# Kernel tuning notes

Measured on AMD Instinct MI355X. Metric: run time of the kernel, lower is better.

Reference implementation:

```python
import jax, jax.numpy as jnp
import numpy as np

IN_F = 4096
OUT_F = 4096
RANK = 16
TOKENS = 8192
WORDS = IN_F // 16  # 16 int2 codes per int32 word
LORA_SCALE = 1.0


def pack_int2(codes):
    """codes: [out_f, in_f] int32 in {0,1,2} -> packed [out_f, in_f//16] int32.
    Little-endian: code k of a word sits at bits [2k, 2k+1]."""
    c = codes.reshape(codes.shape[0], -1, 16)  # [out, words, 16]
    shifts = jnp.arange(16, dtype=jnp.int32) * 2
    return jnp.sum(c << shifts, axis=-1).astype(jnp.int32)


def unpack_int2(packed, in_features):
    """packed: [out_f, words] int32 -> ternary floats [out_f, in_f] in {-1,0,+1}."""
    shifts = jnp.arange(16, dtype=jnp.int32) * 2
    codes = (packed[:, :, None] >> shifts) & 3  # [out, words, 16]
    codes = codes.reshape(packed.shape[0], -1)[:, :in_features]
    return codes - 1  # {0,1,2} -> {-1,0,+1}


def setup_inputs() -> dict:
    key = jax.random.key(0)
    kx, kc, ka, km, kb, kA, kB = jax.random.split(key, 7)
    x = jax.random.normal(kx, (TOKENS, IN_F), dtype=jnp.float32)
    codes = jax.random.randint(kc, (OUT_F, IN_F), 0, 3, dtype=jnp.int32)  # {0,1,2}
    int2_packed = pack_int2(codes)  # [OUT_F, WORDS]
    alpha = jax.random.uniform(ka, (OUT_F,), dtype=jnp.float32) * 0.1 + 0.01
    mu = jax.random.normal(km, (OUT_F,), dtype=jnp.float32) * 0.01
    bias = jax.random.normal(kb, (OUT_F,), dtype=jnp.float32) * 0.02
    lora_A = jax.random.normal(kA, (RANK, IN_F), dtype=jnp.float32) * 0.02
    lora_B = jax.random.normal(kB, (OUT_F, RANK), dtype=jnp.float32) * 0.02
    return {"x": x, "int2_packed": int2_packed, "alpha": alpha, "mu": mu,
            "bias": bias, "lora_A": lora_A, "lora_B": lora_B}


def reference(x, int2_packed, alpha, mu, bias, lora_A, lora_B):
    # Unpack ternary weight T in {-1,0,+1}: [OUT_F, IN_F]
    T = unpack_int2(int2_packed, IN_F).astype(x.dtype)
    # ternary matmul, per-row scale alpha
    out = jnp.einsum('ti,oi->to', x, T) * alpha[None, :]
    # asymmetric shift: mu_o * sum_i x_i
    out = out + mu[None, :] * jnp.sum(x, axis=-1, keepdims=True)
    # LoRA correction: scale * (x A^T) B^T
    lora_out = jnp.einsum('tr,or->to', jnp.einsum('ti,ri->tr', x, lora_A), lora_B)
    out = out + LORA_SCALE * lora_out
    return out + bias[None, :]
```

## Files before the change

kernel.cpp:

```cpp
#include <hip/hip_runtime.h>
#include <stdint.h>

#define IN_F   4096
#define OUT_F  4096
#define TOKENS 8192
#define RANK   16

#define BM 128
#define BN 128
#define BKI 64

typedef unsigned short u16;
typedef __attribute__((ext_vector_type(8))) short bf16x8;
typedef __attribute__((ext_vector_type(4))) float f32x4;
typedef __attribute__((ext_vector_type(4))) int i32x4;

#define GLDS16(g, l) __builtin_amdgcn_global_load_lds( \
    (__attribute__((address_space(1))) void*)(g),      \
    (__attribute__((address_space(3))) void*)(l), 16, 0, 0)

__device__ __forceinline__ int swz_row(int row) {
    return (row & 3) ^ ((row >> 2) & 1);
}

__device__ __forceinline__ u16 bf16bits(float f) {
    unsigned int u = __builtin_bit_cast(unsigned int, f);
    unsigned int lsb = (u >> 16) & 1u;
    u += 0x7fffu + lsb;
    return (u16)(u >> 16);
}

__device__ __forceinline__ unsigned int quant4(float a, float b, float c, float d, float inv) {
    int qa = __float2int_rn(a * inv); qa = max(-127, min(127, qa));
    int qb = __float2int_rn(b * inv); qb = max(-127, min(127, qb));
    int qc = __float2int_rn(c * inv); qc = max(-127, min(127, qc));
    int qd = __float2int_rn(d * inv); qd = max(-127, min(127, qd));
    return (qa & 255) | ((qb & 255) << 8) | ((qc & 255) << 16) | ((qd & 255) << 24);
}

__global__ __launch_bounds__(256) void k_prep(const float* __restrict__ X,
                                              const int* __restrict__ packed,
                                              const float* __restrict__ lA,
                                              const float* __restrict__ lB,
                                              signed char* __restrict__ Xq,
                                              float* __restrict__ sArr,
                                              float* __restrict__ SArr,
                                              signed char* __restrict__ Wq,
                                              u16* __restrict__ Bl,
                                              signed char* __restrict__ Aq,
                                              float* __restrict__ aScale) {
    __shared__ float rs[4], rm[4];
    const int b = blockIdx.x;
    const int tid = threadIdx.x;
    const int lane = tid & 63;
    const int wv = tid >> 6;

    if (b < TOKENS) {
        const int t = b;
        const float4* X4 = (const float4*)(X + (size_t)t * IN_F);
        float4 v[4];
#pragma unroll
        for (int j = 0; j < 4; j++) v[j] = X4[tid * 4 + j];

        float s = 0.f, m = 0.f;
#pragma unroll
        for (int j = 0; j < 4; j++) {
            s += v[j].x + v[j].y + v[j].z + v[j].w;
            m = fmaxf(m, fmaxf(fmaxf(fabsf(v[j].x), fabsf(v[j].y)),
                               fmaxf(fabsf(v[j].z), fabsf(v[j].w))));
        }
#pragma unroll
        for (int off = 32; off > 0; off >>= 1) {
            s += __shfl_down(s, off);
            m = fmaxf(m, __shfl_down(m, off));
        }
        if (lane == 0) { rs[wv] = s; rm[wv] = m; }
        __syncthreads();
        float S = rs[0] + rs[1] + rs[2] + rs[3];
        float M = fmaxf(fmaxf(rm[0], rm[1]), fmaxf(rm[2], rm[3]));
        M = fmaxf(M, 1e-20f);
        if (tid == 0) { SArr[t] = S; sArr[t] = M / 127.0f; }

        float inv = 127.0f / M;
        uint4 o;
        o.x = quant4(v[0].x, v[0].y, v[0].z, v[0].w, inv);
        o.y = quant4(v[1].x, v[1].y, v[1].z, v[1].w, inv);
        o.z = quant4(v[2].x, v[2].y, v[2].z, v[2].w, inv);
        o.w = quant4(v[3].x, v[3].y, v[3].z, v[3].w, inv);
        *(uint4*)(Xq + (size_t)t * IN_F + tid * 16) = o;
    } else if (b < TOKENS + OUT_F * (IN_F / 16) / 256) {
        int idx = (b - TOKENS) * 256 + tid;
        int p = packed[idx];
        uint4 o;
        unsigned int w[4];
#pragma unroll
        for (int g = 0; g < 4; g++) {
            unsigned int word = 0;
#pragma unroll
            for (int j = 0; j < 4; j++) {
                int k = g * 4 + j;
                int bb = ((p >> (2 * k)) & 3) - 1;
                word |= (unsigned int)(bb & 255) << (8 * j);
            }
            w[g] = word;
        }
        o.x = w[0]; o.y = w[1]; o.z = w[2]; o.w = w[3];
        *(uint4*)(Wq + (size_t)idx * 16) = o;
    } else if (b < TOKENS + OUT_F * (IN_F / 16) / 256 + OUT_F / 256) {
        int o = (b - TOKENS - OUT_F * (IN_F / 16) / 256) * 256 + tid;
        const float4* B4 = (const float4*)(lB + (size_t)o * RANK);
        float4 b0 = B4[0], b1 = B4[1], b2 = B4[2], b3 = B4[3];
        union { u16 u[32]; uint4 q[4]; } ob;
        ob.u[0] = bf16bits(b0.x); ob.u[1] = bf16bits(b0.y); ob.u[2] = bf16bits(b0.z); ob.u[3] = bf16bits(b0.w);
        ob.u[4] = bf16bits(b1.x); ob.u[5] = bf16bits(b1.y); ob.u[6] = bf16bits(b1.z); ob.u[7] = bf16bits(b1.w);
        ob.u[8] = bf16bits(b2.x); ob.u[9] = bf16bits(b2.y); ob.u[10] = bf16bits(b2.z); ob.u[11] = bf16bits(b2.w);
        ob.u[12] = bf16bits(b3.x); ob.u[13] = bf16bits(b3.y); ob.u[14] = bf16bits(b3.z); ob.u[15] = bf16bits(b3.w);
#pragma unroll
        for (int k = 16; k < 32; k++) ob.u[k] = 0;
        uint4* dst = (uint4*)(Bl + (size_t)o * 32);
        dst[0] = ob.q[0]; dst[1] = ob.q[1]; dst[2] = ob.q[2]; dst[3] = ob.q[3];
    } else {
        const int r = b - (TOKENS + OUT_F * (IN_F / 16) / 256 + OUT_F / 256);
        const float4* A4 = (const float4*)(lA + (size_t)r * IN_F);
        float4 v[4];
#pragma unroll
        for (int j = 0; j < 4; j++) v[j] = A4[tid * 4 + j];

        float m = 0.f;
#pragma unroll
        for (int j = 0; j < 4; j++)
            m = fmaxf(m, fmaxf(fmaxf(fabsf(v[j].x), fabsf(v[j].y)),
                               fmaxf(fabsf(v[j].z), fabsf(v[j].w))));
#pragma unroll
        for (int off = 32; off > 0; off >>= 1) m = fmaxf(m, __shfl_down(m, off));
        if (lane == 0) rm[wv] = m;
        __syncthreads();
        float M = fmaxf(fmaxf(rm[0], rm[1]), fmaxf(rm[2], rm[3]));
        M = fmaxf(M, 1e-20f);
        if (tid == 0) aScale[r] = M / 127.0f;

        float inv = 127.0f / M;
        uint4 o;
        o.x = quant4(v[0].x, v[0].y, v[0].z, v[0].w, inv);
        o.y = quant4(v[1].x, v[1].y, v[1].z, v[1].w, inv);
        o.z = quant4(v[2].x, v[2].y, v[2].z, v[2].w, inv);
        o.w = quant4(v[3].x, v[3].y, v[3].z, v[3].w, inv);
        *(uint4*)(Aq + (size_t)r * IN_F + tid * 16) = o;
    }
}

__global__ __launch_bounds__(256) void k_lora_y(const signed char* __restrict__ Xq,
                                                const signed char* __restrict__ Aq,
                                                const float* __restrict__ sArr,
                                                const float* __restrict__ aScale,
                                                u16* __restrict__ ypad) {
    __shared__ i32x4 red[4][64];
    const int tid = threadIdx.x;
    const int lane = tid & 63;
    const int wv = tid >> 6;
    const int t0 = blockIdx.x * 16;
    const int fr = lane & 15;
    const int q16 = (lane >> 4) * 16;

    i32x4 acc = {};
    const signed char* xrow = Xq + (size_t)(t0 + fr) * IN_F + wv * 1024 + q16;
    const signed char* arow = Aq + (size_t)fr * IN_F + wv * 1024 + q16;
#pragma unroll
    for (int k0 = 0; k0 < 1024; k0 += BKI) {
        i32x4 af = *(const i32x4*)(xrow + k0);
        i32x4 bf = *(const i32x4*)(arow + k0);
        acc = __builtin_amdgcn_mfma_i32_16x16x64_i8(af, bf, acc, 0, 0, 0);
    }
    red[wv][lane] = acc;
    __syncthreads();
    if (wv == 0) {
        i32x4 s0 = red[0][lane], s1 = red[1][lane], s2 = red[2][lane], s3 = red[3][lane];
        const int c0 = lane & 15;
        const int r0 = (lane >> 4) * 4;
        float asc = aScale[c0];
#pragma unroll
        for (int r = 0; r < 4; r++) {
            int t = t0 + r0 + r;
            float y = sArr[t] * asc * (float)(s0[r] + s1[r] + s2[r] + s3[r]);
            ypad[(size_t)t * 32 + c0] = bf16bits(y);
            ypad[(size_t)t * 32 + 16 + c0] = 0;
        }
    }
}

__global__ __launch_bounds__(256, 2) void k_gemm_i8(const signed char* __restrict__ Xq,
                                                    const signed char* __restrict__ Wq,
                                                    const float* __restrict__ sArr,
                                                    const float* __restrict__ SArr,
                                                    const float* __restrict__ alpha,
                                                    const float* __restrict__ mu,
                                                    const float* __restrict__ bias,
                                                    const u16* __restrict__ ypad,
                                                    const u16* __restrict__ Bl,
                                                    float* __restrict__ out) {
    __shared__ unsigned char smem[16384];
    unsigned char* smA = smem;
    unsigned char* smB = smem + 8192;

    const int tid = threadIdx.x;
    const int lane = tid & 63;
    const int wv = tid >> 6;
    const int wm = (wv >> 1) * 64;
    const int wn = (wv & 1) * 64;
    const int fr = lane & 15;
    const int qs = lane >> 4;
    const int sw = swz_row(fr);
    const int rdoff = ((qs ^ sw) << 4);
    const int wvbase = wv * 1024;

    const int m0 = blockIdx.y * BM;
    const int n0 = blockIdx.x * BN;

    int srow[2], soff[2];
#pragma unroll
    for (int i = 0; i < 2; i++) {
        int c = i * 256 + tid;
        srow[i] = c >> 2;
        soff[i] = (((c & 3) ^ swz_row(c >> 2)) << 4);
    }

    i32x4 acc[4][4] = {};

    for (int k0 = 0; k0 < IN_F; k0 += BKI) {
        __syncthreads();
#pragma unroll
        for (int i = 0; i < 2; i++)
            GLDS16(Xq + (size_t)(m0 + srow[i]) * IN_F + k0 + soff[i], smA + i * 4096 + wvbase);
#pragma unroll
        for (int i = 0; i < 2; i++)
            GLDS16(Wq + (size_t)(n0 + srow[i]) * IN_F + k0 + soff[i], smB + i * 4096 + wvbase);
        __syncthreads();

        i32x4 af[4], bf[4];
#pragma unroll
        for (int mt = 0; mt < 4; mt++)
            af[mt] = *(const i32x4*)(smA + (wm + mt * 16 + fr) * BKI + rdoff);
#pragma unroll
        for (int nt = 0; nt < 4; nt++)
            bf[nt] = *(const i32x4*)(smB + (wn + nt * 16 + fr) * BKI + rdoff);
#pragma unroll
        for (int mt = 0; mt < 4; mt++)
#pragma unroll
            for (int nt = 0; nt < 4; nt++)
                acc[mt][nt] = __builtin_amdgcn_mfma_i32_16x16x64_i8(af[mt], bf[nt], acc[mt][nt], 0, 0, 0);
    }

    const int r0 = (lane >> 4) * 4;
    const int c0 = lane & 15;
    f32x4 facc[4][4];
#pragma unroll
    for (int mt = 0; mt < 4; mt++) {
        int rb = m0 + wm + mt * 16 + r0;
        f32x4 sv = *(const f32x4*)(sArr + rb);
        f32x4 Sv = *(const f32x4*)(SArr + rb);
#pragma unroll
        for (int nt = 0; nt < 4; nt++) {
            int col = n0 + wn + nt * 16 + c0;
            float av = alpha[col], mv = mu[col], bv = bias[col];
#pragma unroll
            for (int r = 0; r < 4; r++)
                facc[mt][nt][r] = av * sv[r] * (float)acc[mt][nt][r] + fmaf(mv, Sv[r], bv);
        }
    }

    __syncthreads();
#pragma unroll
    for (int i = 0; i < 2; i++) {
        GLDS16((const unsigned char*)ypad + (size_t)(m0 + srow[i]) * 64 + soff[i], smA + i * 4096 + wvbase);
        GLDS16((const unsigned char*)Bl + (size_t)(n0 + srow[i]) * 64 + soff[i], smB + i * 4096 + wvbase);
    }
    __syncthreads();
    bf16x8 yf[4], blf[4];
#pragma unroll
    for (int mt = 0; mt < 4; mt++)
        yf[mt] = *(const bf16x8*)(smA + (wm + mt * 16 + fr) * 64 + rdoff);
#pragma unroll
    for (int nt = 0; nt < 4; nt++)
        blf[nt] = *(const bf16x8*)(smB + (wn + nt * 16 + fr) * 64 + rdoff);
#pragma unroll
    for (int mt = 0; mt < 4; mt++)
#pragma unroll
        for (int nt = 0; nt < 4; nt++)
            facc[mt][nt] = __builtin_amdgcn_mfma_f32_16x16x32_bf16(yf[mt], blf[nt], facc[mt][nt], 0, 0, 0);

#pragma unroll
    for (int nt = 0; nt < 4; nt++) {
        int col = n0 + wn + nt * 16 + c0;
#pragma unroll
        for (int mt = 0; mt < 4; mt++) {
            int row = m0 + wm + mt * 16 + r0;
            float* op = out + (size_t)row * OUT_F + col;
#pragma unroll
            for (int r = 0; r < 4; r++)
                op[(size_t)r * OUT_F] = facc[mt][nt][r];
        }
    }
}

extern "C" void kernel_launch(void* const* d_in, const int* in_sizes, int n_in,
                              void* d_out, int out_size, void* d_ws, size_t ws_size,
                              hipStream_t stream) {
    const float* x      = (const float*)d_in[0];
    const int*   packed = (const int*)d_in[1];
    const float* alpha  = (const float*)d_in[2];
    const float* mu     = (const float*)d_in[3];
    const float* bias   = (const float*)d_in[4];
    const float* lA     = (const float*)d_in[5];
    const float* lB     = (const float*)d_in[6];
    float* out = (float*)d_out;

    char* p = (char*)d_ws;
    signed char* Wq = (signed char*)p;             p += (size_t)OUT_F * IN_F;
    signed char* Xq = (signed char*)p;             p += (size_t)TOKENS * IN_F;
    float* sArr = (float*)p;                       p += (size_t)TOKENS * 4;
    float* SArr = (float*)p;                       p += (size_t)TOKENS * 4;
    u16* ypad = (u16*)p;                           p += (size_t)TOKENS * 32 * 2;
    u16* Bl = (u16*)p;                             p += (size_t)OUT_F * 32 * 2;
    signed char* Aq = (signed char*)p;             p += (size_t)RANK * IN_F;
    float* aScale = (float*)p;                     p += RANK * 4;

    const int prep_blocks = TOKENS + OUT_F * (IN_F / 16) / 256 + OUT_F / 256 + RANK;
    k_prep<<<dim3(prep_blocks), dim3(256), 0, stream>>>(x, packed, lA, lB, Xq, sArr, SArr, Wq, Bl, Aq, aScale);
    k_lora_y<<<dim3(TOKENS / 16), dim3(256), 0, stream>>>(Xq, Aq, sArr, aScale, ypad);

    dim3 grid(OUT_F / BN, TOKENS / BM);
    k_gemm_i8<<<grid, dim3(256), 0, stream>>>(Xq, Wq, sArr, SArr, alpha, mu, bias, ypad, Bl, out);
}
```

Baseline: 395.5 us.

## Rewrite int8 GEMM as 256x256 tile, 8-wave, double-buffered ping-pong pipeline

The int8 GEMM moves from 128x128 tiles with a 64-deep K step and single-buffered LDS to 256x256 tiles with a 128-deep K step and 512 threads. It double-buffers 128KB of LDS, splits each K tile into half-tile phases that overlap global-to-LDS loads with MFMA work, and uses explicit vmcnt waits, barriers and setprio. A swizzled 1D grid improves L2 locality. The aim is to hide memory latency and raise MFMA utilisation, at the cost of large LDS use (likely one block per CU despite the launch bound) and more register pressure.

```diff
diff --git a/kernel.cpp b/kernel.cpp
--- a/kernel.cpp
+++ b/kernel.cpp
@@ -6,9 +6,10 @@
 #define TOKENS 8192
 #define RANK   16
 
-#define BM 128
-#define BN 128
-#define BKI 64
+#define BM 256
+#define BN 256
+#define BK 128
+#define NT (IN_F / BK)
 
 typedef unsigned short u16;
 typedef __attribute__((ext_vector_type(8))) short bf16x8;
@@ -19,9 +20,12 @@
     (__attribute__((address_space(1))) void*)(g),      \
     (__attribute__((address_space(3))) void*)(l), 16, 0, 0)
 
-__device__ __forceinline__ int swz_row(int row) {
-    return (row & 3) ^ ((row >> 2) & 1);
-}
+#define MEMFENCE asm volatile("" ::: "memory")
+#define BARRIER  do { MEMFENCE; __builtin_amdgcn_s_barrier(); MEMFENCE; } while (0)
+#define VMCNT8   asm volatile("s_waitcnt vmcnt(8)" ::: "memory")
+#define VMCNT0   asm volatile("s_waitcnt vmcnt(0)" ::: "memory")
+
+__device__ __forceinline__ int swz4(int row) { return (row & 3) ^ ((row >> 2) & 1); }
 
 __device__ __forceinline__ u16 bf16bits(float f) {
     unsigned int u = __builtin_bit_cast(unsigned int, f);
@@ -166,7 +170,7 @@
     const signed char* xrow = Xq + (size_t)(t0 + fr) * IN_F + wv * 1024 + q16;
     const signed char* arow = Aq + (size_t)fr * IN_F + wv * 1024 + q16;
 #pragma unroll
-    for (int k0 = 0; k0 < 1024; k0 += BKI) {
+    for (int k0 = 0; k0 < 1024; k0 += 64) {
         i32x4 af = *(const i32x4*)(xrow + k0);
         i32x4 bf = *(const i32x4*)(arow + k0);
         acc = __builtin_amdgcn_mfma_i32_16x16x64_i8(af, bf, acc, 0, 0, 0);
@@ -188,7 +192,80 @@
     }
 }
 
-__global__ __launch_bounds__(256, 2) void k_gemm_i8(const signed char* __restrict__ Xq,
+
+#define STAGE_A(srcTile, h, dbuf)                                              \
+    {                                                                          \
+        _Pragma("unroll")                                                      \
+        for (int j = 0; j < 2; j++) {                                          \
+            int c = j * 512 + tid;                                             \
+            int rho = c >> 3;                                                  \
+            int sl = (c & 7) ^ (rho & 7);                                      \
+            int trow = ((rho >> 6) << 7) + ((h) << 6) + (rho & 63);            \
+            GLDS16(Xq + (size_t)(m0 + trow) * IN_F + (srcTile) * BK + sl * 16, \
+                   smem + (dbuf) * 65536 + (h) * 16384 + j * 8192 + wvb);      \
+        }                                                                      \
+    }
+
+#define STAGE_B(srcTile, h, dbuf)                                              \
+    {                                                                          \
+        _Pragma("unroll")                                                      \
+        for (int j = 0; j < 2; j++) {                                          \
+            int c = j * 512 + tid;                                             \
+            int rho = c >> 3;                                                  \
+            int sl = (c & 7) ^ (rho & 7);                                      \
+            int tcol = ((rho >> 5) << 6) + ((h) << 5) + (rho & 31);            \
+            GLDS16(Wq + (size_t)(n0 + tcol) * IN_F + (srcTile) * BK + sl * 16, \
+                   smem + (dbuf) * 65536 + 32768 + (h) * 16384 + j * 8192 + wvb); \
+        }                                                                      \
+    }
+
+#define READ_A(h)                                                              \
+    {                                                                          \
+        _Pragma("unroll")                                                      \
+        for (int ml = 0; ml < 4; ml++) {                                       \
+            _Pragma("unroll")                                                  \
+            for (int ks = 0; ks < 2; ks++) {                                   \
+                int rho = wmi * 64 + ml * 16 + fr;                             \
+                int s = (ks * 4 + qs) ^ (rho & 7);                             \
+                af[ml][ks] = *(const i32x4*)(smem + d * 65536 + (h) * 16384 +  \
+                                             rho * 128 + s * 16);              \
+            }                                                                  \
+        }                                                                      \
+    }
+
+#define READ_B(hb)                                                             \
+    {                                                                          \
+        _Pragma("unroll")                                                      \
+        for (int nl = 0; nl < 2; nl++) {                                       \
+            _Pragma("unroll")                                                  \
+            for (int ks = 0; ks < 2; ks++) {                                   \
+                int rho = wni * 32 + nl * 16 + fr;                             \
+                int s = (ks * 4 + qs) ^ (rho & 7);                             \
+                bf[(hb) * 2 + nl][ks] = *(const i32x4*)(smem + d * 65536 +     \
+                    32768 + (hb) * 16384 + rho * 128 + s * 16);                \
+            }                                                                  \
+        }                                                                      \
+    }
+
+#define MFMA_PHASE(ha, hb)                                                     \
+    {                                                                          \
+        __builtin_amdgcn_s_setprio(1);                                         \
+        _Pragma("unroll")                                                      \
+        for (int ml = 0; ml < 4; ml++) {                                       \
+            _Pragma("unroll")                                                  \
+            for (int nl = 0; nl < 2; nl++) {                                   \
+                _Pragma("unroll")                                              \
+                for (int ks = 0; ks < 2; ks++)                                 \
+                    acc[(ha) * 4 + ml][(hb) * 2 + nl] =                        \
+                        __builtin_amdgcn_mfma_i32_16x16x64_i8(                 \
+                            af[ml][ks], bf[(hb) * 2 + nl][ks],                 \
+                            acc[(ha) * 4 + ml][(hb) * 2 + nl], 0, 0, 0);       \
+            }                                                                  \
+        }                                                                      \
+        __builtin_amdgcn_s_setprio(0);                                         \
+    }
+
+__global__ __launch_bounds__(512, 2) void k_gemm_i8(const signed char* __restrict__ Xq,
                                                     const signed char* __restrict__ Wq,
                                                     const float* __restrict__ sArr,
                                                     const float* __restrict__ SArr,
@@ -198,102 +275,115 @@
                                                     const u16* __restrict__ ypad,
                                                     const u16* __restrict__ Bl,
                                                     float* __restrict__ out) {
-    __shared__ unsigned char smem[16384];
-    unsigned char* smA = smem;
-    unsigned char* smB = smem + 8192;
+    __shared__ unsigned char smem[131072];
 
     const int tid = threadIdx.x;
     const int lane = tid & 63;
-    const int wv = tid >> 6;
-    const int wm = (wv >> 1) * 64;
-    const int wn = (wv & 1) * 64;
+    const int wid = tid >> 6;
+    const int wmi = wid >> 2;
+    const int wni = wid & 3;
     const int fr = lane & 15;
     const int qs = lane >> 4;
-    const int sw = swz_row(fr);
-    const int rdoff = ((qs ^ sw) << 4);
-    const int wvbase = wv * 1024;
-
-    const int m0 = blockIdx.y * BM;
-    const int n0 = blockIdx.x * BN;
-
-    int srow[2], soff[2];
-#pragma unroll
-    for (int i = 0; i < 2; i++) {
-        int c = i * 256 + tid;
-        srow[i] = c >> 2;
-        soff[i] = (((c & 3) ^ swz_row(c >> 2)) << 4);
-    }
-
-    i32x4 acc[4][4] = {};
-
-    for (int k0 = 0; k0 < IN_F; k0 += BKI) {
-        __syncthreads();
-#pragma unroll
-        for (int i = 0; i < 2; i++)
-            GLDS16(Xq + (size_t)(m0 + srow[i]) * IN_F + k0 + soff[i], smA + i * 4096 + wvbase);
-#pragma unroll
-        for (int i = 0; i < 2; i++)
-            GLDS16(Wq + (size_t)(n0 + srow[i]) * IN_F + k0 + soff[i], smB + i * 4096 + wvbase);
-        __syncthreads();
-
-        i32x4 af[4], bf[4];
-#pragma unroll
-        for (int mt = 0; mt < 4; mt++)
-            af[mt] = *(const i32x4*)(smA + (wm + mt * 16 + fr) * BKI + rdoff);
-#pragma unroll
-        for (int nt = 0; nt < 4; nt++)
-            bf[nt] = *(const i32x4*)(smB + (wn + nt * 16 + fr) * BKI + rdoff);
-#pragma unroll
-        for (int mt = 0; mt < 4; mt++)
-#pragma unroll
-            for (int nt = 0; nt < 4; nt++)
-                acc[mt][nt] = __builtin_amdgcn_mfma_i32_16x16x64_i8(af[mt], bf[nt], acc[mt][nt], 0, 0, 0);
-    }
-
-    const int r0 = (lane >> 4) * 4;
-    const int c0 = lane & 15;
-    f32x4 facc[4][4];
-#pragma unroll
-    for (int mt = 0; mt < 4; mt++) {
-        int rb = m0 + wm + mt * 16 + r0;
+    const int wvb = wid * 1024;
+
+    int id = blockIdx.x;
+    int swz = (id & 7) * 64 + (id >> 3);
+    const int m0 = (swz >> 4) * BM;
+    const int n0 = (swz & 15) * BN;
+
+    i32x4 acc[8][4] = {};
+    i32x4 af[4][2], bf[4][2];
+
+    STAGE_A(0, 0, 0); STAGE_B(0, 0, 0); STAGE_B(0, 1, 0); STAGE_A(0, 1, 0);
+    STAGE_A(1, 0, 1); STAGE_B(1, 0, 1);
+    VMCNT8; BARRIER;
+
+#pragma unroll 2
+    for (int t = 0; t < NT; ++t) {
+        const int d = t & 1;
+        const int dn = d ^ 1;
+        const int tp1 = (t + 1 < NT) ? (t + 1) : (NT - 1);
+        const int tp2 = (t + 2 < NT) ? (t + 2) : (NT - 1);
+        READ_A(0); READ_B(0);
+        STAGE_B(tp1, 1, dn);
+        VMCNT8; BARRIER;
+        MFMA_PHASE(0, 0);
+        BARRIER;
+        READ_B(1);
+        STAGE_A(tp1, 1, dn);
+        VMCNT8; BARRIER;
+        MFMA_PHASE(0, 1);
+        BARRIER;
+        READ_A(1);
+        STAGE_A(tp2, 0, d);
+        BARRIER;
+        MFMA_PHASE(1, 1);
+        BARRIER;
+        STAGE_B(tp2, 0, d);
+        VMCNT8; BARRIER;
+        MFMA_PHASE(1, 0);
+        BARRIER;
+    }
+
+    VMCNT0; BARRIER;
+#pragma unroll
+    for (int j = 0; j < 2; j++) {
+        int c = j * 512 + tid;
+        int row = c >> 2;
+        int sl = ((c & 3) ^ swz4(row)) << 4;
+        GLDS16((const unsigned char*)ypad + (size_t)(m0 + row) * 64 + sl,
+               smem + j * 8192 + wvb);
+        GLDS16((const unsigned char*)Bl + (size_t)(n0 + row) * 64 + sl,
+               smem + 16384 + j * 8192 + wvb);
+    }
+
+    const int r0 = qs * 4;
+    const int c0 = fr;
+    float av[4], mv[4], bv[4];
+#pragma unroll
+    for (int nt = 0; nt < 4; nt++) {
+        int col = n0 + wni * 64 + nt * 16 + c0;
+        av[nt] = alpha[col]; mv[nt] = mu[col]; bv[nt] = bias[col];
+    }
+    f32x4 facc[8][4];
+#pragma unroll
+    for (int mt = 0; mt < 8; mt++) {
+        int rb = m0 + wmi * 128 + mt * 16 + r0;
         f32x4 sv = *(const f32x4*)(sArr + rb);
         f32x4 Sv = *(const f32x4*)(SArr + rb);
 #pragma unroll
-        for (int nt = 0; nt < 4; nt++) {
-            int col = n0 + wn + nt * 16 + c0;
-            float av = alpha[col], mv = mu[col], bv = bias[col];
+        for (int nt = 0; nt < 4; nt++)
 #pragma unroll
             for (int r = 0; r < 4; r++)
-                facc[mt][nt][r] = av * sv[r] * (float)acc[mt][nt][r] + fmaf(mv, Sv[r], bv);
-        }
-    }
-
-    __syncthreads();
-#pragma unroll
-    for (int i = 0; i < 2; i++) {
-        GLDS16((const unsigned char*)ypad + (size_t)(m0 + srow[i]) * 64 + soff[i], smA + i * 4096 + wvbase);
-        GLDS16((const unsigned char*)Bl + (size_t)(n0 + srow[i]) * 64 + soff[i], smB + i * 4096 + wvbase);
-    }
-    __syncthreads();
-    bf16x8 yf[4], blf[4];
-#pragma unroll
-    for (int mt = 0; mt < 4; mt++)
-        yf[mt] = *(const bf16x8*)(smA + (wm + mt * 16 + fr) * 64 + rdoff);
-#pragma unroll
-    for (int nt = 0; nt < 4; nt++)
-        blf[nt] = *(const bf16x8*)(smB + (wn + nt * 16 + fr) * 64 + rdoff);
-#pragma unroll
-    for (int mt = 0; mt < 4; mt++)
+                facc[mt][nt][r] = av[nt] * sv[r] * (float)acc[mt][nt][r] + fmaf(mv[nt], Sv[r], bv[nt]);
+    }
+
+    VMCNT0; BARRIER;
+    bf16x8 yf[8], blf[4];
+#pragma unroll
+    for (int mt = 0; mt < 8; mt++) {
+        int row = wmi * 128 + mt * 16 + fr;
+        int s = (qs ^ swz4(row)) << 4;
+        yf[mt] = *(const bf16x8*)(smem + row * 64 + s);
+    }
+#pragma unroll
+    for (int nt = 0; nt < 4; nt++) {
+        int row = wni * 64 + nt * 16 + fr;
+        int s = (qs ^ swz4(row)) << 4;
+        blf[nt] = *(const bf16x8*)(smem + 16384 + row * 64 + s);
+    }
+#pragma unroll
+    for (int mt = 0; mt < 8; mt++)
 #pragma unroll
         for (int nt = 0; nt < 4; nt++)
             facc[mt][nt] = __builtin_amdgcn_mfma_f32_16x16x32_bf16(yf[mt], blf[nt], facc[mt][nt], 0, 0, 0);
 
 #pragma unroll
-    for (int nt = 0; nt < 4; nt++) {
-        int col = n0 + wn + nt * 16 + c0;
-#pragma unroll
-        for (int mt = 0; mt < 4; mt++) {
-            int row = m0 + wm + mt * 16 + r0;
+    for (int mt = 0; mt < 8; mt++) {
+        int row = m0 + wmi * 128 + mt * 16 + r0;
+#pragma unroll
+        for (int nt = 0; nt < 4; nt++) {
+            int col = n0 + wni * 64 + nt * 16 + c0;
             float* op = out + (size_t)row * OUT_F + col;
 #pragma unroll
             for (int r = 0; r < 4; r++)
@@ -328,6 +418,5 @@
     k_prep<<<dim3(prep_blocks), dim3(256), 0, stream>>>(x, packed, lA, lB, Xq, sArr, SArr, Wq, Bl, Aq, aScale);
     k_lora_y<<<dim3(TOKENS / 16), dim3(256), 0, stream>>>(Xq, Aq, sArr, aScale, ypad);
 
-    dim3 grid(OUT_F / BN, TOKENS / BM);
-    k_gemm_i8<<<grid, dim3(256), 0, stream>>>(Xq, Wq, sArr, SArr, alpha, mu, bias, ypad, Bl, out);
-}
+    k_gemm_i8<<<dim3(512), dim3(512), 0, stream>>>(Xq, Wq, sArr, SArr, alpha, mu, bias, ypad, Bl, out);
+}
```

Result: faster. 363.4 us (-8.1%).
